# Optimization experiments

Measured on AMD Instinct MI355X. Metric: run time of the kernel, lower is better.

## Reference

```python
import jax, jax.numpy as jnp
import numpy as np

N, E = 50000, 400000
F_IN, HID, OUT, H = 128, 64, 40, 4
SLOPE = 0.2


def setup_inputs() -> dict:
    key = jax.random.key(0)
    ks = jax.random.split(key, 20)

    def gn(k, shape, scale=0.05):
        return jax.random.normal(k, shape, dtype=jnp.float32) * scale

    inp = {
        "node_inputs": jax.random.normal(ks[0], (N, F_IN), dtype=jnp.float32),
        "src": jax.random.randint(ks[1], (E,), 0, N),
        "dst": jax.random.randint(ks[2], (E,), 0, N),
    }
    # (in_dim, per-head out_dim) per layer; residual linear only when in != heads*out
    dims = [(F_IN, HID), (H * HID, HID), (H * HID, OUT)]
    i = 3
    for l, (fin, d) in enumerate(dims):
        inp[f"w_src{l}"] = gn(ks[i], (fin, H * d)); i += 1
        inp[f"b_src{l}"] = jnp.zeros((H * d,), jnp.float32)
        inp[f"w_dst{l}"] = gn(ks[i], (fin, H * d)); i += 1
        inp[f"b_dst{l}"] = jnp.zeros((H * d,), jnp.float32)
        inp[f"attn{l}"] = gn(ks[i], (H, d)); i += 1
        if fin != H * d:
            inp[f"w_res{l}"] = gn(ks[i], (fin, H * d)); i += 1
            inp[f"b_res{l}"] = jnp.zeros((H * d,), jnp.float32)
    return inp


def _gatv2_layer(x, src, dst, w_s, b_s, w_d, b_d, attn, res):
    # x: [N, F]; res: [N, H*D] residual term (already projected or identity)
    n = x.shape[0]
    h, d = attn.shape
    hs = (x @ w_s + b_s).reshape(n, h, d)   # feat_src
    hd = (x @ w_d + b_d).reshape(n, h, d)   # feat_dst
    e = hs[src] + hd[dst]                    # [E, H, D]
    e = jnp.where(e > 0, e, SLOPE * e)       # LeakyReLU
    logits = jnp.einsum('ehd,hd->eh', e, attn)  # [E, H]
    # edge softmax over incoming edges of each dst node
    m = jax.ops.segment_max(logits, dst, num_segments=n)
    z = jnp.exp(logits - m[dst])
    s = jax.ops.segment_sum(z, dst, num_segments=n)
    a = z / s[dst]                            # [E, H]
    out = jax.ops.segment_sum(hs[src] * a[:, :, None], dst, num_segments=n)  # [N, H, D]
    return out + res.reshape(n, h, d)


def reference(node_inputs, src, dst,
              w_src0, b_src0, w_dst0, b_dst0, attn0, w_res0, b_res0,
              w_src1, b_src1, w_dst1, b_dst1, attn1,
              w_src2, b_src2, w_dst2, b_dst2, attn2, w_res2, b_res2):
    x = node_inputs
    # layer 0: in=128 != heads*hid -> linear residual
    x = _gatv2_layer(x, src, dst, w_src0, b_src0, w_dst0, b_dst0, attn0,
                     x @ w_res0 + b_res0)
    x = x.reshape(x.shape[0], -1)  # flatten heads
    # layer 1: in == heads*hid -> identity residual
    x = _gatv2_layer(x, src, dst, w_src1, b_src1, w_dst1, b_dst1, attn1, x)
    x = x.reshape(x.shape[0], -1)
    # layer 2: in=256 != heads*out -> linear residual
    x = _gatv2_layer(x, src, dst, w_src2, b_src2, w_dst2, b_dst2, attn2,
                     x @ w_res2 + b_res2)
    # mean over heads: [N, H, OUT] -> [N, OUT]
    return x.mean(axis=-2)
```

## Files before the change

kernel.cpp:

```cpp
#include <hip/hip_runtime.h>
#include <hip/hip_bf16.h>
#include <math.h>

#define SLOPE 0.2f

typedef unsigned short bf16_t;
typedef short bh8 __attribute__((ext_vector_type(8)));
typedef unsigned short us8 __attribute__((ext_vector_type(8)));
typedef float f32x4 __attribute__((ext_vector_type(4)));

__device__ __forceinline__ float bf2f(bf16_t x) {
    return __uint_as_float((unsigned)x << 16);
}
__device__ __forceinline__ bf16_t f2bf(float v) {
    unsigned u = __float_as_uint(v);
    return (bf16_t)((u + 0x7FFFu + ((u >> 16) & 1u)) >> 16);
}
__device__ __forceinline__ ushort2 pk_f2bf(float a, float b) {
    __hip_bfloat162 h2 = __float22bfloat162_rn(float2{a, b});
    union { __hip_bfloat162 h; ushort2 u; } u;
    u.h = h2;
    return u.u;
}


__global__ void hist_dst(const int* __restrict__ dst, int E, int* __restrict__ deg) {
    int e = blockIdx.x * 256 + threadIdx.x;
    if (e < E) atomicAdd(&deg[dst[e]], 1);
}

__global__ void deg_chunk_sum(const int* __restrict__ deg, int n, int* __restrict__ chunk_sums) {
    __shared__ int sm[256];
    int base = blockIdx.x * 1024;
    int s = 0;
    for (int i = threadIdx.x; i < 1024; i += 256) {
        int idx = base + i;
        if (idx < n) s += deg[idx];
    }
    sm[threadIdx.x] = s;
    __syncthreads();
    for (int off = 128; off > 0; off >>= 1) {
        if (threadIdx.x < off) sm[threadIdx.x] += sm[threadIdx.x + off];
        __syncthreads();
    }
    if (threadIdx.x == 0) chunk_sums[blockIdx.x] = sm[0];
}

__global__ void scan_chunk_sums(int* __restrict__ chunk_sums, int nchunks) {
    __shared__ int sm[256];
    int t = threadIdx.x;
    if (t < nchunks) sm[t] = chunk_sums[t];
    __syncthreads();
    if (t == 0) {
        int run = 0;
        for (int i = 0; i < nchunks; i++) { int v = sm[i]; sm[i] = run; run += v; }
    }
    __syncthreads();
    if (t < nchunks) chunk_sums[t] = sm[t];
}

__global__ void scan_write(const int* __restrict__ deg, int n,
                           const int* __restrict__ chunk_sums,
                           int* __restrict__ row_start, int Etot) {
    int base = blockIdx.x * 1024;
    int t = threadIdx.x;
    int v[4];
    int tsum = 0;
#pragma unroll
    for (int j = 0; j < 4; j++) {
        int idx = base + t * 4 + j;
        v[j] = (idx < n) ? deg[idx] : 0;
        tsum += v[j];
    }
    __shared__ int sm[256];
    sm[t] = tsum;
    __syncthreads();
    for (int off = 1; off < 256; off <<= 1) {
        int x = (t >= off) ? sm[t - off] : 0;
        __syncthreads();
        sm[t] += x;
        __syncthreads();
    }
    int excl = sm[t] - tsum + chunk_sums[blockIdx.x];
#pragma unroll
    for (int j = 0; j < 4; j++) {
        int idx = base + t * 4 + j;
        if (idx < n) row_start[idx] = excl;
        excl += v[j];
    }
    if (blockIdx.x == 0 && t == 0) row_start[n] = Etot;
}

__global__ void scatter_edges(const int* __restrict__ dst, const int* __restrict__ src, int E,
                              const int* __restrict__ row_start,
                              int* __restrict__ fill, int* __restrict__ src_sorted) {
    int e = blockIdx.x * 256 + threadIdx.x;
    if (e < E) {
        int d_ = dst[e];
        int pos = row_start[d_] + atomicAdd(&fill[d_], 1);
        src_sorted[pos] = src[e];
    }
}


__global__ void convert_weights(
    const float* __restrict__ w0, const float* __restrict__ w1, const float* __restrict__ w2,
    const float* __restrict__ w3, const float* __restrict__ w4,
    const float* __restrict__ w5, const float* __restrict__ w6,
    const float* __restrict__ wr2, const float* __restrict__ br2,
    bf16_t* __restrict__ t0, bf16_t* __restrict__ t1, bf16_t* __restrict__ t2,
    bf16_t* __restrict__ t3, bf16_t* __restrict__ t4,
    bf16_t* __restrict__ t5, bf16_t* __restrict__ t6,
    bf16_t* __restrict__ teff, float* __restrict__ b_eff)
{
    int b = blockIdx.x, t = threadIdx.x;
    const float* W; bf16_t* T; int K, Nc, lb;
    if (b < 384) {
        int g = b / 128; lb = b - g * 128;
        W = g == 0 ? w0 : (g == 1 ? w1 : w2);
        T = g == 0 ? t0 : (g == 1 ? t1 : t2);
        K = 128; Nc = 256;
    } else if (b < 896) {
        int g = (b - 384) / 256; lb = (b - 384) - g * 256;
        W = g == 0 ? w3 : w4; T = g == 0 ? t3 : t4;
        K = 256; Nc = 256;
    } else if (b < 1280) {
        int g = (b - 896) / 192; lb = (b - 896) - g * 192;
        W = g == 0 ? w5 : w6; T = g == 0 ? t5 : t6;
        K = 256; Nc = 160;
    } else {
        lb = b - 1280;
        int idx = lb * 256 + t;
        int n = idx >> 8, k = idx & 255;
        float v = 0.f;
        if (n < 40)
            v = 0.25f * (wr2[(size_t)k * 160 + n] + wr2[(size_t)k * 160 + 40 + n] +
                         wr2[(size_t)k * 160 + 80 + n] + wr2[(size_t)k * 160 + 120 + n]);
        teff[idx] = f2bf(v);
        if (lb == 0 && t < 40)
            b_eff[t] = 0.25f * (br2[t] + br2[40 + t] + br2[80 + t] + br2[120 + t]);
        return;
    }
    int idx = lb * 256 + t;
    int n = idx / K, k = idx - n * K;
    float v = (n < Nc) ? W[(size_t)k * Nc + n] : 0.f;
    T[idx] = f2bf(v);
}


template <typename TA, int NOUT, int KTOT, int NPAD, bool SPLIT40, bool HAS_EFF>
__global__ __launch_bounds__(256) void gemm_lds(
    const TA* __restrict__ A,
    const bf16_t* __restrict__ Wt0, const bf16_t* __restrict__ Wt1, const bf16_t* __restrict__ Wt2,
    const float* __restrict__ bias0, const float* __restrict__ bias1, const float* __restrict__ bias2,
    bf16_t* __restrict__ C0, bf16_t* __restrict__ C1, bf16_t* __restrict__ C2,
    const bf16_t* __restrict__ Wte, const float* __restrict__ biase, float* __restrict__ Ce,
    int M, int Nc)
{
    constexpr int LSTR = KTOT + 8;
    constexpr int ESTR = 38;
    __shared__ bf16_t As[64 * LSTR];
    __shared__ bf16_t Ep[4 * 64 * ESTR];

    int tid = threadIdx.x;
    int lane = tid & 63, w = tid >> 6;
    int lm = lane & 15, lq = lane >> 4;
    int m0 = blockIdx.x * 64;

    const bf16_t* Wts[3] = {Wt0, Wt1, Wt2};
    const float* biases[3] = {bias0, bias1, bias2};
    bf16_t* Cs[3] = {C0, C1, C2};

    if (sizeof(TA) == 4) {
#pragma unroll
        for (int it = 0; it < 4; it++) {
            int idx = tid + it * 256;
            int r = idx >> 4, c = idx & 15;
            int gm = m0 + r; if (gm >= M) gm = M - 1;
            const float* ap = (const float*)A + (size_t)gm * KTOT + c * 8;
            float4 lo = *(const float4*)ap;
            float4 hi = *(const float4*)(ap + 4);
            ushort2 p0 = pk_f2bf(lo.x, lo.y), p1 = pk_f2bf(lo.z, lo.w);
            ushort2 p2 = pk_f2bf(hi.x, hi.y), p3 = pk_f2bf(hi.z, hi.w);
            bh8 v = { (short)p0.x, (short)p0.y, (short)p1.x, (short)p1.y,
                      (short)p2.x, (short)p2.y, (short)p3.x, (short)p3.y };
            *(bh8*)(As + r * LSTR + c * 8) = v;
        }
    } else {
#pragma unroll
        for (int it = 0; it < 8; it++) {
            int idx = tid + it * 256;
            int r = idx >> 5, c = idx & 31;
            int gm = m0 + r; if (gm >= M) gm = M - 1;
            bh8 v = *(const bh8*)((const bf16_t*)A + (size_t)gm * KTOT + c * 8);
            *(bh8*)(As + r * LSTR + c * 8) = v;
        }
    }
    __syncthreads();

    bf16_t* ep = Ep + w * (64 * ESTR);
    constexpr int NCHUNK = (NPAD + 127) / 128;

#pragma unroll
    for (int chunk = 0; chunk < NCHUNK; chunk++) {
        int n0 = chunk * 128 + w * 32;
        if (n0 >= NPAD) continue;

        int boff[NOUT][2];
#pragma unroll
        for (int o = 0; o < NOUT; o++)
#pragma unroll
            for (int nt = 0; nt < 2; nt++)
                boff[o][nt] = (n0 + nt * 16 + lm) * KTOT + lq * 8;

        f32x4 acc[NOUT][4][2];
#pragma unroll
        for (int o = 0; o < NOUT; o++)
#pragma unroll
            for (int i = 0; i < 4; i++)
#pragma unroll
                for (int j = 0; j < 2; j++)
                    acc[o][i][j] = (f32x4){0.f, 0.f, 0.f, 0.f};

#pragma unroll
        for (int kc = 0; kc < KTOT / 32; kc++) {
            bh8 af[4];
#pragma unroll
            for (int mt = 0; mt < 4; mt++)
                af[mt] = *(const bh8*)(As + (mt * 16 + lm) * LSTR + kc * 32 + lq * 8);
#pragma unroll
            for (int o = 0; o < NOUT; o++) {
                bh8 bf[2];
#pragma unroll
                for (int nt = 0; nt < 2; nt++)
                    bf[nt] = *(const bh8*)(Wts[o] + boff[o][nt] + kc * 32);
#pragma unroll
                for (int mt = 0; mt < 4; mt++)
#pragma unroll
                    for (int nt = 0; nt < 2; nt++)
                        acc[o][mt][nt] = __builtin_amdgcn_mfma_f32_16x16x32_bf16(af[mt], bf[nt], acc[o][mt][nt], 0, 0, 0);
            }
        }

#pragma unroll
        for (int o = 0; o < NOUT; o++) {
#pragma unroll
            for (int nt = 0; nt < 2; nt++) {
                int gn = n0 + nt * 16 + lm;
                float bv = (gn < Nc) ? biases[o][gn] : 0.f;
#pragma unroll
                for (int mt = 0; mt < 4; mt++)
#pragma unroll
                    for (int r = 0; r < 4; r++)
                        ep[(mt * 16 + lq * 4 + r) * ESTR + nt * 16 + lm] = f2bf(acc[o][mt][nt][r] + bv);
            }
#pragma unroll
            for (int it = 0; it < 4; it++) {
                int row = it * 16 + (lane >> 2);
                int cc = (lane & 3) * 8;
                bh8 v = *(const bh8*)(ep + row * ESTR + cc);
                int gm = m0 + row;
                int cg = n0 + cc;
                if (gm < M && cg < Nc) {
                    size_t cb = SPLIT40 ? (size_t)(cg + 24 * (cg / 40)) : (size_t)cg;
                    size_t rs = SPLIT40 ? 256 : (size_t)Nc;
                    *(bh8*)(Cs[o] + (size_t)gm * rs + cb) = v;
                }
            }
        }
    }

    if (HAS_EFF && w < 2) {
        int beoff[2];
#pragma unroll
        for (int nt = 0; nt < 2; nt++)
            beoff[nt] = (w * 32 + nt * 16 + lm) * KTOT + lq * 8;
        f32x4 acc_e[4][2];
#pragma unroll
        for (int i = 0; i < 4; i++)
#pragma unroll
            for (int j = 0; j < 2; j++)
                acc_e[i][j] = (f32x4){0.f, 0.f, 0.f, 0.f};
#pragma unroll
        for (int kc = 0; kc < KTOT / 32; kc++) {
            bh8 af[4];
#pragma unroll
            for (int mt = 0; mt < 4; mt++)
                af[mt] = *(const bh8*)(As + (mt * 16 + lm) * LSTR + kc * 32 + lq * 8);
            bh8 be[2];
#pragma unroll
            for (int nt = 0; nt < 2; nt++)
                be[nt] = *(const bh8*)(Wte + beoff[nt] + kc * 32);
#pragma unroll
            for (int mt = 0; mt < 4; mt++)
#pragma unroll
                for (int nt = 0; nt < 2; nt++)
                    acc_e[mt][nt] = __builtin_amdgcn_mfma_f32_16x16x32_bf16(af[mt], be[nt], acc_e[mt][nt], 0, 0, 0);
        }
#pragma unroll
        for (int nt = 0; nt < 2; nt++) {
            int gn = w * 32 + nt * 16 + lm;
            if (gn >= 40) continue;
            float bv = biase[gn];
#pragma unroll
            for (int mt = 0; mt < 4; mt++)
#pragma unroll
                for (int r = 0; r < 4; r++) {
                    int gm = m0 + mt * 16 + lq * 4 + r;
                    if (gm < M) Ce[(size_t)gm * 40 + gn] = acc_e[mt][nt][r] + bv;
                }
        }
    }
}


__device__ __forceinline__ void chain_update8(float logit, const float h[8],
                                              float& m, float& l, float* a) {
    if (logit > m) {
        float sc = __expf(m - logit);
        l = l * sc + 1.f;
#pragma unroll
        for (int j = 0; j < 8; j++) a[j] = a[j] * sc + h[j];
        m = logit;
    } else {
        float p = __expf(logit - m);
        l += p;
#pragma unroll
        for (int j = 0; j < 8; j++) a[j] += p * h[j];
    }
}

__device__ __forceinline__ float edge_logit8(const float h[8], const float hdf[8], const float at[8]) {
    float p = 0.f;
#pragma unroll
    for (int j = 0; j < 8; j++) {
        float q = h[j] + hdf[j];
        float lr = fmaxf(q, SLOPE * q);
        p += lr * at[j];
    }
    p += __shfl_xor(p, 1, 64);
    p += __shfl_xor(p, 2, 64);
    p += __shfl_xor(p, 4, 64);
    return p;
}

__device__ __forceinline__ void us8_to_f(const us8 v, float* h) {
#pragma unroll
    for (int j = 0; j < 8; j++) h[j] = bf2f(v[j]);
}

template <int DVALID, bool FINAL, bool RES_INPLACE>
__global__ __launch_bounds__(256) void gat_agg_half(
    const bf16_t* __restrict__ hs, const bf16_t* __restrict__ hd,
    const float* __restrict__ attn,
    const int* __restrict__ row_start, const int* __restrict__ src_sorted,
    bf16_t* __restrict__ P, float* __restrict__ out_final, int N)
{
    int w = threadIdx.x >> 6, lane = threadIdx.x & 63;
    int half = lane >> 5, hl = lane & 31;
    int n = blockIdx.x * 8 + w * 2 + half;
    if (n >= N) return;
    int f0 = hl * 8;
    int h = hl >> 3;
    int dp = (hl & 7) * 8;

    float at[8], hdf[8];
#pragma unroll
    for (int j = 0; j < 8; j++)
        at[j] = (dp + j < DVALID) ? attn[h * DVALID + dp + j] : 0.f;
    us8 hv = *(const us8*)(hd + (unsigned)(n * 256 + f0));
    us8_to_f(hv, hdf);

    int s = row_start[n], e = row_start[n + 1];

    float cm[4] = {-INFINITY, -INFINITY, -INFINITY, -INFINITY};
    float cl[4] = {0.f, 0.f, 0.f, 0.f};
    float ca[4][8] = {};

    int i = s;
    for (; i + 4 <= e; i += 4) {
        int sn0 = src_sorted[i], sn1 = src_sorted[i + 1];
        int sn2 = src_sorted[i + 2], sn3 = src_sorted[i + 3];
        us8 r0 = *(const us8*)(hs + (unsigned)(sn0 * 256 + f0));
        us8 r1 = *(const us8*)(hs + (unsigned)(sn1 * 256 + f0));
        us8 r2 = *(const us8*)(hs + (unsigned)(sn2 * 256 + f0));
        us8 r3 = *(const us8*)(hs + (unsigned)(sn3 * 256 + f0));
        float h0[8], h1[8], h2[8], h3[8];
        us8_to_f(r0, h0); us8_to_f(r1, h1); us8_to_f(r2, h2); us8_to_f(r3, h3);
        float p0 = edge_logit8(h0, hdf, at);
        float p1 = edge_logit8(h1, hdf, at);
        float p2 = edge_logit8(h2, hdf, at);
        float p3 = edge_logit8(h3, hdf, at);
        chain_update8(p0, h0, cm[0], cl[0], ca[0]);
        chain_update8(p1, h1, cm[1], cl[1], ca[1]);
        chain_update8(p2, h2, cm[2], cl[2], ca[2]);
        chain_update8(p3, h3, cm[3], cl[3], ca[3]);
    }
    for (; i < e; i++) {
        int sn0 = src_sorted[i];
        us8 r0 = *(const us8*)(hs + (unsigned)(sn0 * 256 + f0));
        float h0[8];
        us8_to_f(r0, h0);
        float p0 = edge_logit8(h0, hdf, at);
        chain_update8(p0, h0, cm[0], cl[0], ca[0]);
    }

    float v[8] = {};
    if (e > s) {
        float M = fmaxf(fmaxf(cm[0], cm[1]), fmaxf(cm[2], cm[3]));
        float L = 0.f;
#pragma unroll
        for (int c = 0; c < 4; c++) {
            float sc = __expf(cm[c] - M);
            L += sc * cl[c];
#pragma unroll
            for (int j = 0; j < 8; j++) v[j] += sc * ca[c][j];
        }
        float inv = 1.f / L;
#pragma unroll
        for (int j = 0; j < 8; j++) v[j] *= inv;
    }

    if (FINAL) {
#pragma unroll
        for (int j = 0; j < 8; j++) {
            v[j] += __shfl_xor(v[j], 8, 64);
            v[j] += __shfl_xor(v[j], 16, 64);
        }
        if (hl < DVALID / 8 + 1 && h == 0 && dp < DVALID) {
            float* op = out_final + (unsigned)(n * DVALID + dp);
            float4 c0 = *(float4*)op;
            float4 c1 = *(float4*)(op + 4);
            c0.x += 0.25f * v[0]; c0.y += 0.25f * v[1];
            c0.z += 0.25f * v[2]; c0.w += 0.25f * v[3];
            c1.x += 0.25f * v[4]; c1.y += 0.25f * v[5];
            c1.z += 0.25f * v[6]; c1.w += 0.25f * v[7];
            *(float4*)op = c0;
            *(float4*)(op + 4) = c1;
        }
    } else {
        unsigned oi = (unsigned)(n * 256 + f0);
        if (RES_INPLACE) {
            us8 pv = *(const us8*)(P + oi);
#pragma unroll
            for (int j = 0; j < 8; j++) v[j] += bf2f(pv[j]);
        }
        us8 ov;
#pragma unroll
        for (int j = 0; j < 8; j++) ov[j] = f2bf(v[j]);
        *(us8*)(P + oi) = ov;
    }
}


extern "C" void kernel_launch(void* const* d_in, const int* in_sizes, int n_in,
                              void* d_out, int out_size, void* d_ws, size_t ws_size,
                              hipStream_t stream) {
    const float* x0    = (const float*)d_in[0];
    const int*   src   = (const int*)d_in[1];
    const int*   dst   = (const int*)d_in[2];
    const float* w_src0 = (const float*)d_in[3];  const float* b_src0 = (const float*)d_in[4];
    const float* w_dst0 = (const float*)d_in[5];  const float* b_dst0 = (const float*)d_in[6];
    const float* attn0  = (const float*)d_in[7];
    const float* w_res0 = (const float*)d_in[8];  const float* b_res0 = (const float*)d_in[9];
    const float* w_src1 = (const float*)d_in[10]; const float* b_src1 = (const float*)d_in[11];
    const float* w_dst1 = (const float*)d_in[12]; const float* b_dst1 = (const float*)d_in[13];
    const float* attn1  = (const float*)d_in[14];
    const float* w_src2 = (const float*)d_in[15]; const float* b_src2 = (const float*)d_in[16];
    const float* w_dst2 = (const float*)d_in[17]; const float* b_dst2 = (const float*)d_in[18];
    const float* attn2  = (const float*)d_in[19];
    const float* w_res2 = (const float*)d_in[20]; const float* b_res2 = (const float*)d_in[21];

    const int N = in_sizes[0] / 128;
    const int E = in_sizes[1];
    float* out = (float*)d_out;
    (void)n_in; (void)out_size; (void)ws_size;

    char* ws = (char*)d_ws;
    size_t off = 0;
    auto alloc = [&](size_t bytes) {
        void* q = ws + off;
        off = (off + bytes + 255) & ~(size_t)255;
        return q;
    };
    int* deg        = (int*)alloc((size_t)2 * N * 4);
    int* fill       = deg + N;
    int* row_start  = (int*)alloc((size_t)(N + 1) * 4);
    int* chunk_sums = (int*)alloc(256 * 4);
    int* src_sorted = (int*)alloc((size_t)E * 4);
    bf16_t* t_src0 = (bf16_t*)alloc(256 * 128 * 2);
    bf16_t* t_dst0 = (bf16_t*)alloc(256 * 128 * 2);
    bf16_t* t_res0 = (bf16_t*)alloc(256 * 128 * 2);
    bf16_t* t_src1 = (bf16_t*)alloc(256 * 256 * 2);
    bf16_t* t_dst1 = (bf16_t*)alloc(256 * 256 * 2);
    bf16_t* t_src2 = (bf16_t*)alloc(192 * 256 * 2);
    bf16_t* t_dst2 = (bf16_t*)alloc(192 * 256 * 2);
    bf16_t* t_eff  = (bf16_t*)alloc(64 * 256 * 2);
    float*  b_eff  = (float*)alloc(64 * 4);
    const size_t elems = (size_t)N * 256;
    bf16_t* P  = (bf16_t*)alloc(elems * 2);
    bf16_t* HS = (bf16_t*)alloc(elems * 2);
    bf16_t* HD = (bf16_t*)alloc(elems * 2);

    hipMemsetAsync(deg, 0, (size_t)2 * N * 4, stream);
    int eblocks = (E + 255) / 256;
    int nchunks = (N + 1023) / 1024;
    hipLaunchKernelGGL(hist_dst, dim3(eblocks), dim3(256), 0, stream, dst, E, deg);
    hipLaunchKernelGGL(convert_weights, dim3(1344), dim3(256), 0, stream,
                       w_src0, w_dst0, w_res0, w_src1, w_dst1, w_src2, w_dst2, w_res2, b_res2,
                       t_src0, t_dst0, t_res0, t_src1, t_dst1, t_src2, t_dst2, t_eff, b_eff);
    hipLaunchKernelGGL(deg_chunk_sum, dim3(nchunks), dim3(256), 0, stream, deg, N, chunk_sums);
    hipLaunchKernelGGL(scan_chunk_sums, dim3(1), dim3(256), 0, stream, chunk_sums, nchunks);
    hipLaunchKernelGGL(scan_write, dim3(nchunks), dim3(256), 0, stream, deg, N, chunk_sums, row_start, E);
    hipLaunchKernelGGL(scatter_edges, dim3(eblocks), dim3(256), 0, stream, dst, src, E, row_start, fill, src_sorted);

    dim3 blk(256);
    int mtiles = (N + 63) / 64;
    int ab = (N + 7) / 8;

    hipLaunchKernelGGL((gemm_lds<float, 3, 128, 256, false, false>), dim3(mtiles), blk, 0, stream,
                       x0, t_src0, t_dst0, t_res0, b_src0, b_dst0, b_res0,
                       HS, HD, P,
                       (const bf16_t*)nullptr, (const float*)nullptr, (float*)nullptr,
                       N, 256);
    hipLaunchKernelGGL((gat_agg_half<64, false, true>), dim3(ab), blk, 0, stream,
                       HS, HD, attn0, row_start, src_sorted, P, (float*)nullptr, N);

    hipLaunchKernelGGL((gemm_lds<bf16_t, 2, 256, 256, false, false>), dim3(mtiles), blk, 0, stream,
                       P, t_src1, t_dst1, (const bf16_t*)nullptr, b_src1, b_dst1, (const float*)nullptr,
                       HS, HD, (bf16_t*)nullptr,
                       (const bf16_t*)nullptr, (const float*)nullptr, (float*)nullptr,
                       N, 256);
    hipLaunchKernelGGL((gat_agg_half<64, false, true>), dim3(ab), blk, 0, stream,
                       HS, HD, attn1, row_start, src_sorted, P, (float*)nullptr, N);

    hipLaunchKernelGGL((gemm_lds<bf16_t, 2, 256, 192, true, true>), dim3(mtiles), blk, 0, stream,
                       P, t_src2, t_dst2, (const bf16_t*)nullptr, b_src2, b_dst2, (const float*)nullptr,
                       HS, HD, (bf16_t*)nullptr,
                       t_eff, b_eff, out,
                       N, 160);
    hipLaunchKernelGGL((gat_agg_half<40, true, false>), dim3(ab), blk, 0, stream,
                       HS, HD, attn2, row_start, src_sorted, (bf16_t*)nullptr, out, N);
}
```

Measured before the change: 455.2 us.

## Swizzle GEMM LDS tile, store MFMA output directly, single-kernel degree scan

The GEMM's A tile in LDS now uses an XOR swizzle instead of row padding. The MFMA operands are swapped so each lane holds four consecutive output columns, which lets the epilogue write results straight to global memory with packed 8-byte stores. This removes the LDS staging buffer and its extra round trip. The three-kernel degree prefix scan is replaced by one 1024-thread block, cutting two launches but serialising the scan on a single CU. The aggregation guard condition is also simplified.

Result: slower. 556.2 us (+22.2%).

```diff
diff --git a/kernel.cpp b/kernel.cpp
--- a/kernel.cpp
+++ b/kernel.cpp
@@ -29,66 +29,33 @@
     if (e < E) atomicAdd(&deg[dst[e]], 1);
 }
 
-__global__ void deg_chunk_sum(const int* __restrict__ deg, int n, int* __restrict__ chunk_sums) {
-    __shared__ int sm[256];
-    int base = blockIdx.x * 1024;
+__global__ __launch_bounds__(1024) void scan_single(const int* __restrict__ deg, int n, int chunk,
+                                                    int* __restrict__ row_start, int Etot) {
+    __shared__ int sm[1024];
+    int t = threadIdx.x;
+    int base = t * chunk;
     int s = 0;
-    for (int i = threadIdx.x; i < 1024; i += 256) {
+    for (int i = 0; i < chunk; i++) {
         int idx = base + i;
         if (idx < n) s += deg[idx];
     }
-    sm[threadIdx.x] = s;
+    sm[t] = s;
     __syncthreads();
-    for (int off = 128; off > 0; off >>= 1) {
-        if (threadIdx.x < off) sm[threadIdx.x] += sm[threadIdx.x + off];
-        __syncthreads();
-    }
-    if (threadIdx.x == 0) chunk_sums[blockIdx.x] = sm[0];
-}
-
-__global__ void scan_chunk_sums(int* __restrict__ chunk_sums, int nchunks) {
-    __shared__ int sm[256];
-    int t = threadIdx.x;
-    if (t < nchunks) sm[t] = chunk_sums[t];
-    __syncthreads();
-    if (t == 0) {
-        int run = 0;
-        for (int i = 0; i < nchunks; i++) { int v = sm[i]; sm[i] = run; run += v; }
-    }
-    __syncthreads();
-    if (t < nchunks) chunk_sums[t] = sm[t];
-}
-
-__global__ void scan_write(const int* __restrict__ deg, int n,
-                           const int* __restrict__ chunk_sums,
-                           int* __restrict__ row_start, int Etot) {
-    int base = blockIdx.x * 1024;
-    int t = threadIdx.x;
-    int v[4];
-    int tsum = 0;
-#pragma unroll
-    for (int j = 0; j < 4; j++) {
-        int idx = base + t * 4 + j;
-        v[j] = (idx < n) ? deg[idx] : 0;
-        tsum += v[j];
-    }
-    __shared__ int sm[256];
-    sm[t] = tsum;
-    __syncthreads();
-    for (int off = 1; off < 256; off <<= 1) {
+    for (int off = 1; off < 1024; off <<= 1) {
         int x = (t >= off) ? sm[t - off] : 0;
         __syncthreads();
         sm[t] += x;
         __syncthreads();
     }
-    int excl = sm[t] - tsum + chunk_sums[blockIdx.x];
-#pragma unroll
-    for (int j = 0; j < 4; j++) {
-        int idx = base + t * 4 + j;
-        if (idx < n) row_start[idx] = excl;
-        excl += v[j];
-    }
-    if (blockIdx.x == 0 && t == 0) row_start[n] = Etot;
+    int excl = sm[t] - s;
+    for (int i = 0; i < chunk; i++) {
+        int idx = base + i;
+        if (idx < n) {
+            row_start[idx] = excl;
+            excl += deg[idx];
+        }
+    }
+    if (t == 0) row_start[n] = Etot;
 }
 
 __global__ void scatter_edges(const int* __restrict__ dst, const int* __restrict__ src, int E,
@@ -149,7 +116,7 @@
 
 
 template <typename TA, int NOUT, int KTOT, int NPAD, bool SPLIT40, bool HAS_EFF>
-__global__ __launch_bounds__(256) void gemm_lds(
+__global__ __launch_bounds__(256) void gemm_swz(
     const TA* __restrict__ A,
     const bf16_t* __restrict__ Wt0, const bf16_t* __restrict__ Wt1, const bf16_t* __restrict__ Wt2,
     const float* __restrict__ bias0, const float* __restrict__ bias1, const float* __restrict__ bias2,
@@ -157,10 +124,7 @@
     const bf16_t* __restrict__ Wte, const float* __restrict__ biase, float* __restrict__ Ce,
     int M, int Nc)
 {
-    constexpr int LSTR = KTOT + 8;
-    constexpr int ESTR = 38;
-    __shared__ bf16_t As[64 * LSTR];
-    __shared__ bf16_t Ep[4 * 64 * ESTR];
+    __shared__ bf16_t As[64 * KTOT];
 
     int tid = threadIdx.x;
     int lane = tid & 63, w = tid >> 6;
@@ -184,7 +148,7 @@
             ushort2 p2 = pk_f2bf(hi.x, hi.y), p3 = pk_f2bf(hi.z, hi.w);
             bh8 v = { (short)p0.x, (short)p0.y, (short)p1.x, (short)p1.y,
                       (short)p2.x, (short)p2.y, (short)p3.x, (short)p3.y };
-            *(bh8*)(As + r * LSTR + c * 8) = v;
+            *(bh8*)(As + r * KTOT + ((c ^ (r & 7)) * 8)) = v;
         }
     } else {
 #pragma unroll
@@ -193,12 +157,12 @@
             int r = idx >> 5, c = idx & 31;
             int gm = m0 + r; if (gm >= M) gm = M - 1;
             bh8 v = *(const bh8*)((const bf16_t*)A + (size_t)gm * KTOT + c * 8);
-            *(bh8*)(As + r * LSTR + c * 8) = v;
+            *(bh8*)(As + r * KTOT + ((c ^ (r & 7)) * 8)) = v;
         }
     }
     __syncthreads();
 
-    bf16_t* ep = Ep + w * (64 * ESTR);
+    int swz = lm & 7;
     constexpr int NCHUNK = (NPAD + 127) / 128;
 
 #pragma unroll
@@ -227,7 +191,7 @@
             bh8 af[4];
 #pragma unroll
             for (int mt = 0; mt < 4; mt++)
-                af[mt] = *(const bh8*)(As + (mt * 16 + lm) * LSTR + kc * 32 + lq * 8);
+                af[mt] = *(const bh8*)(As + (mt * 16 + lm) * KTOT + (((kc * 4 + lq) ^ swz) * 8));
 #pragma unroll
             for (int o = 0; o < NOUT; o++) {
                 bh8 bf[2];
@@ -238,7 +202,7 @@
                 for (int mt = 0; mt < 4; mt++)
 #pragma unroll
                     for (int nt = 0; nt < 2; nt++)
-                        acc[o][mt][nt] = __builtin_amdgcn_mfma_f32_16x16x32_bf16(af[mt], bf[nt], acc[o][mt][nt], 0, 0, 0);
+                        acc[o][mt][nt] = __builtin_amdgcn_mfma_f32_16x16x32_bf16(bf[nt], af[mt], acc[o][mt][nt], 0, 0, 0);
             }
         }
 
@@ -246,25 +210,20 @@
         for (int o = 0; o < NOUT; o++) {
 #pragma unroll
             for (int nt = 0; nt < 2; nt++) {
-                int gn = n0 + nt * 16 + lm;
-                float bv = (gn < Nc) ? biases[o][gn] : 0.f;
-#pragma unroll
-                for (int mt = 0; mt < 4; mt++)
-#pragma unroll
-                    for (int r = 0; r < 4; r++)
-                        ep[(mt * 16 + lq * 4 + r) * ESTR + nt * 16 + lm] = f2bf(acc[o][mt][nt][r] + bv);
-            }
-#pragma unroll
-            for (int it = 0; it < 4; it++) {
-                int row = it * 16 + (lane >> 2);
-                int cc = (lane & 3) * 8;
-                bh8 v = *(const bh8*)(ep + row * ESTR + cc);
-                int gm = m0 + row;
-                int cg = n0 + cc;
-                if (gm < M && cg < Nc) {
-                    size_t cb = SPLIT40 ? (size_t)(cg + 24 * (cg / 40)) : (size_t)cg;
-                    size_t rs = SPLIT40 ? 256 : (size_t)Nc;
-                    *(bh8*)(Cs[o] + (size_t)gm * rs + cb) = v;
+                int nb = n0 + nt * 16 + lq * 4;
+                if (nb >= Nc) continue;
+                float4 bv = *(const float4*)(biases[o] + nb);
+                int cb = SPLIT40 ? (nb + 24 * (nb / 40)) : nb;
+                size_t rs = SPLIT40 ? 256 : (size_t)Nc;
+#pragma unroll
+                for (int mt = 0; mt < 4; mt++) {
+                    int gm = m0 + mt * 16 + lm;
+                    if (gm >= M) continue;
+                    f32x4 av = acc[o][mt][nt];
+                    ushort2 lo = pk_f2bf(av[0] + bv.x, av[1] + bv.y);
+                    ushort2 hi = pk_f2bf(av[2] + bv.z, av[3] + bv.w);
+                    ushort4 st = {lo.x, lo.y, hi.x, hi.y};
+                    *(ushort4*)(Cs[o] + (size_t)gm * rs + cb) = st;
                 }
             }
         }
@@ -286,7 +245,7 @@
             bh8 af[4];
 #pragma unroll
             for (int mt = 0; mt < 4; mt++)
-                af[mt] = *(const bh8*)(As + (mt * 16 + lm) * LSTR + kc * 32 + lq * 8);
+                af[mt] = *(const bh8*)(As + (mt * 16 + lm) * KTOT + (((kc * 4 + lq) ^ swz) * 8));
             bh8 be[2];
 #pragma unroll
             for (int nt = 0; nt < 2; nt++)
@@ -295,20 +254,21 @@
             for (int mt = 0; mt < 4; mt++)
 #pragma unroll
                 for (int nt = 0; nt < 2; nt++)
-                    acc_e[mt][nt] = __builtin_amdgcn_mfma_f32_16x16x32_bf16(af[mt], be[nt], acc_e[mt][nt], 0, 0, 0);
+                    acc_e[mt][nt] = __builtin_amdgcn_mfma_f32_16x16x32_bf16(be[nt], af[mt], acc_e[mt][nt], 0, 0, 0);
         }
 #pragma unroll
         for (int nt = 0; nt < 2; nt++) {
-            int gn = w * 32 + nt * 16 + lm;
-            if (gn >= 40) continue;
-            float bv = biase[gn];
-#pragma unroll
-            for (int mt = 0; mt < 4; mt++)
-#pragma unroll
-                for (int r = 0; r < 4; r++) {
-                    int gm = m0 + mt * 16 + lq * 4 + r;
-                    if (gm < M) Ce[(size_t)gm * 40 + gn] = acc_e[mt][nt][r] + bv;
-                }
+            int nb = w * 32 + nt * 16 + lq * 4;
+            if (nb >= 40) continue;
+            float4 bv = *(const float4*)(biase + nb);
+#pragma unroll
+            for (int mt = 0; mt < 4; mt++) {
+                int gm = m0 + mt * 16 + lm;
+                if (gm >= M) continue;
+                f32x4 av = acc_e[mt][nt];
+                float4 st = {av[0] + bv.x, av[1] + bv.y, av[2] + bv.z, av[3] + bv.w};
+                *(float4*)(Ce + (size_t)gm * 40 + nb) = st;
+            }
         }
     }
 }
@@ -427,7 +387,7 @@
             v[j] += __shfl_xor(v[j], 8, 64);
             v[j] += __shfl_xor(v[j], 16, 64);
         }
-        if (hl < DVALID / 8 + 1 && h == 0 && dp < DVALID) {
+        if (h == 0 && dp < DVALID) {
             float* op = out_final + (unsigned)(n * DVALID + dp);
             float4 c0 = *(float4*)op;
             float4 c1 = *(float4*)(op + 4);
@@ -486,7 +446,6 @@
     int* deg        = (int*)alloc((size_t)2 * N * 4);
     int* fill       = deg + N;
     int* row_start  = (int*)alloc((size_t)(N + 1) * 4);
-    int* chunk_sums = (int*)alloc(256 * 4);
     int* src_sorted = (int*)alloc((size_t)E * 4);
     bf16_t* t_src0 = (bf16_t*)alloc(256 * 128 * 2);
     bf16_t* t_dst0 = (bf16_t*)alloc(256 * 128 * 2);
@@ -504,21 +463,19 @@
 
     hipMemsetAsync(deg, 0, (size_t)2 * N * 4, stream);
     int eblocks = (E + 255) / 256;
-    int nchunks = (N + 1023) / 1024;
     hipLaunchKernelGGL(hist_dst, dim3(eblocks), dim3(256), 0, stream, dst, E, deg);
     hipLaunchKernelGGL(convert_weights, dim3(1344), dim3(256), 0, stream,
                        w_src0, w_dst0, w_res0, w_src1, w_dst1, w_src2, w_dst2, w_res2, b_res2,
                        t_src0, t_dst0, t_res0, t_src1, t_dst1, t_src2, t_dst2, t_eff, b_eff);
-    hipLaunchKernelGGL(deg_chunk_sum, dim3(nchunks), dim3(256), 0, stream, deg, N, chunk_sums);
-    hipLaunchKernelGGL(scan_chunk_sums, dim3(1), dim3(256), 0, stream, chunk_sums, nchunks);
-    hipLaunchKernelGGL(scan_write, dim3(nchunks), dim3(256), 0, stream, deg, N, chunk_sums, row_start, E);
+    hipLaunchKernelGGL(scan_single, dim3(1), dim3(1024), 0, stream,
+                       deg, N, (N + 1023) / 1024, row_start, E);
     hipLaunchKernelGGL(scatter_edges, dim3(eblocks), dim3(256), 0, stream, dst, src, E, row_start, fill, src_sorted);
 
     dim3 blk(256);
     int mtiles = (N + 63) / 64;
     int ab = (N + 7) / 8;
 
-    hipLaunchKernelGGL((gemm_lds<float, 3, 128, 256, false, false>), dim3(mtiles), blk, 0, stream,
+    hipLaunchKernelGGL((gemm_swz<float, 3, 128, 256, false, false>), dim3(mtiles), blk, 0, stream,
                        x0, t_src0, t_dst0, t_res0, b_src0, b_dst0, b_res0,
                        HS, HD, P,
                        (const bf16_t*)nullptr, (const float*)nullptr, (float*)nullptr,
@@ -526,7 +483,7 @@
     hipLaunchKernelGGL((gat_agg_half<64, false, true>), dim3(ab), blk, 0, stream,
                        HS, HD, attn0, row_start, src_sorted, P, (float*)nullptr, N);
 
-    hipLaunchKernelGGL((gemm_lds<bf16_t, 2, 256, 256, false, false>), dim3(mtiles), blk, 0, stream,
+    hipLaunchKernelGGL((gemm_swz<bf16_t, 2, 256, 256, false, false>), dim3(mtiles), blk, 0, stream,
                        P, t_src1, t_dst1, (const bf16_t*)nullptr, b_src1, b_dst1, (const float*)nullptr,
                        HS, HD, (bf16_t*)nullptr,
                        (const bf16_t*)nullptr, (const float*)nullptr, (float*)nullptr,
@@ -534,7 +491,7 @@
     hipLaunchKernelGGL((gat_agg_half<64, false, true>), dim3(ab), blk, 0, stream,
                        HS, HD, attn1, row_start, src_sorted, P, (float*)nullptr, N);
 
-    hipLaunchKernelGGL((gemm_lds<bf16_t, 2, 256, 192, true, true>), dim3(mtiles), blk, 0, stream,
+    hipLaunchKernelGGL((gemm_swz<bf16_t, 2, 256, 192, true, true>), dim3(mtiles), blk, 0, stream,
                        P, t_src2, t_dst2, (const bf16_t*)nullptr, b_src2, b_dst2, (const float*)nullptr,
                        HS, HD, (bf16_t*)nullptr,
                        t_eff, b_eff, out,
```
